# Kernel tuning notes

Hardware: AMD Instinct MI355X
Metric: run time of the kernel (lower is better)

## Reference

```python
import jax, jax.numpy as jnp
import numpy as np

B, S, D, P, W = 16, 100, 8192, 100, 3  # batch, seq, feat dim, proj width, window size


def setup_inputs() -> dict:
    key = jax.random.key(0)
    ks = jax.random.split(key, 6)
    return {
        "x": jax.random.normal(ks[0], (B, S, D), dtype=jnp.float32),
        "wq": jax.random.normal(ks[1], (D, P), dtype=jnp.float32) * (1.0 / np.sqrt(D)),
        "wk": jax.random.normal(ks[2], (D, P), dtype=jnp.float32) * (1.0 / np.sqrt(D)),
        "wv": jax.random.normal(ks[3], (D, P), dtype=jnp.float32) * (1.0 / np.sqrt(D)),
        "forwardpad": jax.random.normal(ks[4], (B, 1, D), dtype=jnp.float32),
        "backwardpad": jax.random.normal(ks[5], (B, 1, D), dtype=jnp.float32),
    }


def reference(x, wq, wk, wv, forwardpad, backwardpad):
    # pad: (B, S+2, D)
    padded = jnp.concatenate([forwardpad, x, backwardpad], axis=1)
    # gather all 100 overlapping size-3 windows at once: (B, S, W, D)
    idx = jnp.arange(S)[:, None] + jnp.arange(W)[None, :]  # (S, W)
    windows = padded[:, idx, :]
    # shared projections across all windows (original recomputed per window)
    q = jnp.einsum("bswd,dp->bswp", windows, wq)
    k = jnp.einsum("bswd,dp->bswp", windows, wk)
    v = jnp.einsum("bswd,dp->bswp", windows, wv)
    # per-window 3x3 attention
    scores = jnp.einsum("bswp,bsup->bswu", q, k)  # (B, S, W, W)
    attn = jax.nn.softmax(scores, axis=-1)
    out = jnp.einsum("bswu,bsup->bswp", attn, v)  # (B, S, W, P)
    # original concatenates windows along seq then takes [:, 1::3, :] -> center token of each window
    return out[:, :, 1, :]  # (B, S, P)
```

## Files before the change

kernel.cpp:

```cpp
#include <hip/hip_runtime.h>
#include <hip/hip_bf16.h>
#include <hip/hip_fp16.h>

constexpr int Dk   = 8192;
constexpr int Bb   = 16;
constexpr int Ss   = 100;
constexpr int Pp   = 100;
constexpr int MROW = 1632;
constexpr int NT   = 20;
constexpr int NCC  = 320;
constexpr int NQ   = 304;
constexpr int KG   = 1024;
constexpr int KC   = 16;
constexpr int CH   = 5;
constexpr int MBL  = 52;

constexpr size_t B_SEG   = (size_t)NT * KG * 128;
constexpr size_t PSTRIDE = (size_t)1664 * NCC;

typedef short s8v __attribute__((ext_vector_type(8)));
typedef short s4v __attribute__((ext_vector_type(4)));
typedef float f4v __attribute__((ext_vector_type(4)));

__device__ inline unsigned short f2bf_rne(float f) {
    unsigned u = __float_as_uint(f);
    u += 0x7fffu + ((u >> 16) & 1u);
    return (unsigned short)(u >> 16);
}

__global__ __launch_bounds__(256) void pack_b(
    const float* __restrict__ wq, const float* __restrict__ wk,
    const float* __restrict__ wv,
    short* __restrict__ b_hi, short* __restrict__ b_lo) {
    const int id = blockIdx.x * 256 + threadIdx.x;
    const int n  = id % NCC;
    const int kg = id / NCC;
    if (kg >= KG) return;

    const float* w = nullptr; int p = 0;
    if (n < 100)      { w = wq; p = n; }
    else if (n < 200) { w = wk; p = n - 100; }
    else if (n < 300) { w = wv; p = n - 200; }

    s8v hi, lo;
    #pragma unroll
    for (int j = 0; j < 8; ++j) {
        const float v = w ? w[(size_t)(kg * 8 + j) * Pp + p] : 0.0f;
        const unsigned u = __float_as_uint(v);
        hi[j] = (short)(unsigned short)(u >> 16);
        const float hf = __uint_as_float(u & 0xffff0000u);
        lo[j] = (short)f2bf_rne(v - hf);
    }
    const size_t doff = ((size_t)(n >> 4) * KG + kg) * 128 + (size_t)(n & 15) * 8;
    *(s8v*)(b_hi + doff) = hi;
    *(s8v*)(b_lo + doff) = lo;
}

__global__ __launch_bounds__(256, 2) void qkv_gemm(
    const float* __restrict__ x, const float* __restrict__ fpad,
    const float* __restrict__ bpad,
    const short* __restrict__ b_hi, const short* __restrict__ b_lo,
    unsigned short* __restrict__ part) {
    __shared__ __align__(16) short ahis[2][1024];
    __shared__ __align__(16) short alos[2][1024];

    const int mb   = blockIdx.x;
    const int kc   = blockIdx.y;
    const int tid  = threadIdx.x;
    const int w    = tid >> 6;
    const int l    = tid & 63;
    const int m    = l & 15;
    const int quad = l >> 4;

    const int sr  = tid >> 3;
    const int skq = tid & 7;
    const float* sp;
    {
        const int r = mb * 32 + sr;
        if (r >= MROW) sp = fpad;
        else {
            const int b = r / 102, rr = r - b * 102;
            if (rr == 0)        sp = fpad + (size_t)b * Dk;
            else if (rr == 101) sp = bpad + (size_t)b * Dk;
            else                sp = x + ((size_t)b * Ss + (rr - 1)) * Dk;
        }
        sp += kc * 512 + skq * 4;
    }
    const int woff = ((sr >> 4) * 4 + (skq >> 1)) * 128 + (sr & 15) * 8 + (skq & 1) * 4;

    float4 av[4];
    #pragma unroll
    for (int p = 0; p < 4; ++p) av[p] = *(const float4*)(sp + p * 32);

    s8v bh[2][5], bl[2][5];
    {
        const int kg0 = kc * 64 + quad;
        #pragma unroll
        for (int j = 0; j < 5; ++j) {
            const size_t bo = ((size_t)(w * 5 + j) * KG + kg0) * 128 + (size_t)m * 8;
            bh[0][j] = *(const s8v*)(b_hi + bo);
            bl[0][j] = *(const s8v*)(b_lo + bo);
        }
    }

    f4v acc[2][5];
    #pragma unroll
    for (int i = 0; i < 2; ++i)
        #pragma unroll
        for (int j = 0; j < 5; ++j) {
            f4v z = {0.f, 0.f, 0.f, 0.f};
            acc[i][j] = z;
        }

    #pragma unroll
    for (int s = 0; s < 16; ++s) {
        const int cur = s & 1, nxt = cur ^ 1;

        if (s < 15) {
            const int kgn = kc * 64 + (s + 1) * 4 + quad;
            #pragma unroll
            for (int j = 0; j < 5; ++j) {
                const size_t bo = ((size_t)(w * 5 + j) * KG + kgn) * 128 + (size_t)m * 8;
                bh[nxt][j] = *(const s8v*)(b_hi + bo);
                bl[nxt][j] = *(const s8v*)(b_lo + bo);
            }
        }

        const float4 va = av[s & 3];
        const float vv[4] = {va.x, va.y, va.z, va.w};
        s4v h4, l4;
        #pragma unroll
        for (int jj = 0; jj < 4; ++jj) {
            const unsigned u = __float_as_uint(vv[jj]);
            h4[jj] = (short)(unsigned short)(u >> 16);
            l4[jj] = (short)f2bf_rne(vv[jj] - __uint_as_float(u & 0xffff0000u));
        }
        if (s < 12) av[s & 3] = *(const float4*)(sp + (s + 4) * 32);

        *(s4v*)&ahis[cur][woff] = h4;
        *(s4v*)&alos[cur][woff] = l4;
        __syncthreads();

        const s8v ah0 = *(const s8v*)&ahis[cur][(quad * 16 + m) * 8];
        const s8v ah1 = *(const s8v*)&ahis[cur][((4 + quad) * 16 + m) * 8];
        const s8v al0 = *(const s8v*)&alos[cur][(quad * 16 + m) * 8];
        const s8v al1 = *(const s8v*)&alos[cur][((4 + quad) * 16 + m) * 8];

        #pragma unroll
        for (int j = 0; j < 5; ++j) {
            const s8v bhv = bh[cur][j], blv = bl[cur][j];
            acc[0][j] = __builtin_amdgcn_mfma_f32_16x16x32_bf16(ah0, bhv, acc[0][j], 0, 0, 0);
            acc[1][j] = __builtin_amdgcn_mfma_f32_16x16x32_bf16(ah1, bhv, acc[1][j], 0, 0, 0);
            acc[0][j] = __builtin_amdgcn_mfma_f32_16x16x32_bf16(al0, bhv, acc[0][j], 0, 0, 0);
            acc[1][j] = __builtin_amdgcn_mfma_f32_16x16x32_bf16(al1, bhv, acc[1][j], 0, 0, 0);
            acc[0][j] = __builtin_amdgcn_mfma_f32_16x16x32_bf16(ah0, blv, acc[0][j], 0, 0, 0);
            acc[1][j] = __builtin_amdgcn_mfma_f32_16x16x32_bf16(ah1, blv, acc[1][j], 0, 0, 0);
        }
    }

    unsigned short* __restrict__ pout = part + (size_t)kc * PSTRIDE;
    #pragma unroll
    for (int i = 0; i < 2; ++i) {
        #pragma unroll
        for (int j = 0; j < 5; ++j) {
            const int col  = (w * 5 + j) * 16 + m;
            const int row0 = mb * 32 + i * 16 + quad * 4;
            #pragma unroll
            for (int r = 0; r < 4; ++r)
                pout[(size_t)(row0 + r) * NCC + col] =
                    __half_as_ushort(__float2half(acc[i][j][r]));
        }
    }
}

__global__ __launch_bounds__(256) void reduce_k(
    const unsigned short* __restrict__ part, float* __restrict__ qkv) {
    const int t = blockIdx.x * 256 + threadIdx.x;
    const int row = t / 40;
    const int col0 = (t - row * 40) * 8;
    const size_t base = (size_t)row * NCC + col0;

    float sum[8] = {0.f, 0.f, 0.f, 0.f, 0.f, 0.f, 0.f, 0.f};
    #pragma unroll
    for (int k = 0; k < KC; ++k) {
        const s8v u = *(const s8v*)(part + (size_t)k * PSTRIDE + base);
        #pragma unroll
        for (int ii = 0; ii < 8; ++ii)
            sum[ii] += __half2float(__ushort_as_half((unsigned short)u[ii]));
    }
    if (col0 < NQ) {
        f4v a = {sum[0], sum[1], sum[2], sum[3]};
        f4v b = {sum[4], sum[5], sum[6], sum[7]};
        *(f4v*)(qkv + (size_t)row * NQ + col0)     = a;
        *(f4v*)(qkv + (size_t)row * NQ + col0 + 4) = b;
    }
}

__global__ __launch_bounds__(256) void attn3(
    const float* __restrict__ qkv, float* __restrict__ out) {
    const int blk = blockIdx.x;
    const int b  = blk / (Ss / CH);
    const int c  = blk % (Ss / CH);
    const int s0 = c * CH;
    const int tid = threadIdx.x;

    __shared__ float red[CH + 2][304];
    __shared__ float sc[CH][3];

    for (int idx = tid; idx < (CH + 2) * 300; idx += 256) {
        const int row = idx / 300, col = idx % 300;
        red[row][col] = qkv[(size_t)(b * 102 + s0 + row) * NQ + col];
    }
    __syncthreads();

    if (tid < CH * 3 * 16) {
        const int d = tid >> 4, g = tid & 15;
        const int ss = d / 3, u = d % 3;
        float ps = 0.0f;
        #pragma unroll
        for (int t = 0; t < 7; ++t) {
            const int p = g + t * 16;
            if (p < Pp) ps += red[ss + 1][p] * red[ss + u][100 + p];
        }
        #pragma unroll
        for (int off = 8; off > 0; off >>= 1) ps += __shfl_down(ps, off, 16);
        if (g == 0) sc[ss][u] = ps;
    }
    __syncthreads();

    for (int idx = tid; idx < CH * Pp; idx += 256) {
        const int ss = idx / Pp, p = idx % Pp;
        const float a0 = sc[ss][0], a1 = sc[ss][1], a2 = sc[ss][2];
        const float mx = fmaxf(a0, fmaxf(a1, a2));
        const float e0 = __expf(a0 - mx), e1 = __expf(a1 - mx), e2 = __expf(a2 - mx);
        const float inv = 1.0f / (e0 + e1 + e2);
        out[(size_t)(b * Ss + s0 + ss) * Pp + p] =
            inv * (e0 * red[ss][200 + p] + e1 * red[ss + 1][200 + p] +
                   e2 * red[ss + 2][200 + p]);
    }
}

extern "C" void kernel_launch(void* const* d_in, const int* in_sizes, int n_in,
                              void* d_out, int out_size, void* d_ws, size_t ws_size,
                              hipStream_t stream) {
    const float* x    = (const float*)d_in[0];
    const float* wq   = (const float*)d_in[1];
    const float* wk   = (const float*)d_in[2];
    const float* wv   = (const float*)d_in[3];
    const float* fpad = (const float*)d_in[4];
    const float* bpad = (const float*)d_in[5];
    float* out = (float*)d_out;

    short* b_hi = (short*)d_ws;
    short* b_lo = b_hi + B_SEG;
    unsigned short* part = (unsigned short*)(b_lo + B_SEG);
    float* qkv = (float*)(part + (size_t)KC * PSTRIDE);

    pack_b<<<(NCC * KG) / 256, 256, 0, stream>>>(wq, wk, wv, b_hi, b_lo);
    qkv_gemm<<<dim3(MBL, KC), 256, 0, stream>>>(x, fpad, bpad, b_hi, b_lo, part);
    reduce_k<<<260, 256, 0, stream>>>(part, qkv);
    attn3<<<Bb * (Ss / CH), 256, 0, stream>>>(qkv, out);
}
```

Baseline: 141.5 us.

## Vectorize weight packing, batch GEMM A staging, split reduction across lanes

pack_b now has each thread load float4s and pack four output columns, which cuts scalar global loads. qkv_gemm stages four K-steps of A into a larger LDS buffer per barrier, so it syncs less often, and it loads B fragments directly instead of double-buffering them in registers. reduce_k splits the 16-way K reduction across 4 lanes and combines them with xor shuffles, giving more threads and more memory parallelism. attn3 loads qkv with float4. The trade-offs are higher LDS use in the GEMM and the loss of B prefetch overlap.

```diff
diff --git a/kernel.cpp b/kernel.cpp
--- a/kernel.cpp
+++ b/kernel.cpp
@@ -33,27 +33,42 @@
     const float* __restrict__ wv,
     short* __restrict__ b_hi, short* __restrict__ b_lo) {
     const int id = blockIdx.x * 256 + threadIdx.x;
-    const int n  = id % NCC;
-    const int kg = id / NCC;
+    const int ng = id % 80;
+    const int kg = id / 80;
     if (kg >= KG) return;
-
-    const float* w = nullptr; int p = 0;
-    if (n < 100)      { w = wq; p = n; }
-    else if (n < 200) { w = wk; p = n - 100; }
-    else if (n < 300) { w = wv; p = n - 200; }
-
-    s8v hi, lo;
+    const int n0 = ng * 4;
+
+    const float* w = nullptr; int p0 = 0;
+    if (n0 < 100)      { w = wq; p0 = n0; }
+    else if (n0 < 200) { w = wk; p0 = n0 - 100; }
+    else if (n0 < 300) { w = wv; p0 = n0 - 200; }
+
+    float4 vj[8];
     #pragma unroll
     for (int j = 0; j < 8; ++j) {
-        const float v = w ? w[(size_t)(kg * 8 + j) * Pp + p] : 0.0f;
-        const unsigned u = __float_as_uint(v);
-        hi[j] = (short)(unsigned short)(u >> 16);
-        const float hf = __uint_as_float(u & 0xffff0000u);
-        lo[j] = (short)f2bf_rne(v - hf);
-    }
-    const size_t doff = ((size_t)(n >> 4) * KG + kg) * 128 + (size_t)(n & 15) * 8;
-    *(s8v*)(b_hi + doff) = hi;
-    *(s8v*)(b_lo + doff) = lo;
+        if (w) vj[j] = *(const float4*)(w + (size_t)(kg * 8 + j) * Pp + p0);
+        else   vj[j] = make_float4(0.f, 0.f, 0.f, 0.f);
+    }
+
+    #pragma unroll
+    for (int t = 0; t < 4; ++t) {
+        const int n = n0 + t;
+        const float vv[8] = {vj[0].x + 0.f, vj[1].x, vj[2].x, vj[3].x,
+                             vj[4].x, vj[5].x, vj[6].x, vj[7].x};
+        s8v hi, lo;
+        #pragma unroll
+        for (int j = 0; j < 8; ++j) {
+            const float v = (t == 0) ? (&vj[j].x)[0] : (t == 1) ? (&vj[j].x)[1]
+                          : (t == 2) ? (&vj[j].x)[2] : (&vj[j].x)[3];
+            const unsigned u = __float_as_uint(v);
+            hi[j] = (short)(unsigned short)(u >> 16);
+            lo[j] = (short)f2bf_rne(v - __uint_as_float(u & 0xffff0000u));
+        }
+        (void)vv;
+        const size_t doff = ((size_t)(n >> 4) * KG + kg) * 128 + (size_t)(n & 15) * 8;
+        *(s8v*)(b_hi + doff) = hi;
+        *(s8v*)(b_lo + doff) = lo;
+    }
 }
 
 __global__ __launch_bounds__(256, 2) void qkv_gemm(
@@ -61,8 +76,8 @@
     const float* __restrict__ bpad,
     const short* __restrict__ b_hi, const short* __restrict__ b_lo,
     unsigned short* __restrict__ part) {
-    __shared__ __align__(16) short ahis[2][1024];
-    __shared__ __align__(16) short alos[2][1024];
+    __shared__ __align__(16) short ahis[2][4096];
+    __shared__ __align__(16) short alos[2][4096];
 
     const int mb   = blockIdx.x;
     const int kc   = blockIdx.y;
@@ -88,21 +103,6 @@
     }
     const int woff = ((sr >> 4) * 4 + (skq >> 1)) * 128 + (sr & 15) * 8 + (skq & 1) * 4;
 
-    float4 av[4];
-    #pragma unroll
-    for (int p = 0; p < 4; ++p) av[p] = *(const float4*)(sp + p * 32);
-
-    s8v bh[2][5], bl[2][5];
-    {
-        const int kg0 = kc * 64 + quad;
-        #pragma unroll
-        for (int j = 0; j < 5; ++j) {
-            const size_t bo = ((size_t)(w * 5 + j) * KG + kg0) * 128 + (size_t)m * 8;
-            bh[0][j] = *(const s8v*)(b_hi + bo);
-            bl[0][j] = *(const s8v*)(b_lo + bo);
-        }
-    }
-
     f4v acc[2][5];
     #pragma unroll
     for (int i = 0; i < 2; ++i)
@@ -112,50 +112,58 @@
             acc[i][j] = z;
         }
 
-    #pragma unroll
-    for (int s = 0; s < 16; ++s) {
-        const int cur = s & 1, nxt = cur ^ 1;
-
-        if (s < 15) {
-            const int kgn = kc * 64 + (s + 1) * 4 + quad;
+    float4 avA[4];
+    #pragma unroll
+    for (int st = 0; st < 4; ++st) avA[st] = *(const float4*)(sp + st * 32);
+
+    #pragma unroll
+    for (int g = 0; g < 4; ++g) {
+        const int buf = g & 1;
+
+        #pragma unroll
+        for (int st = 0; st < 4; ++st) {
+            const float vv[4] = {avA[st].x, avA[st].y, avA[st].z, avA[st].w};
+            s4v h4, l4;
+            #pragma unroll
+            for (int jj = 0; jj < 4; ++jj) {
+                const unsigned u = __float_as_uint(vv[jj]);
+                h4[jj] = (short)(unsigned short)(u >> 16);
+                l4[jj] = (short)f2bf_rne(vv[jj] - __uint_as_float(u & 0xffff0000u));
+            }
+            *(s4v*)&ahis[buf][st * 1024 + woff] = h4;
+            *(s4v*)&alos[buf][st * 1024 + woff] = l4;
+        }
+        __syncthreads();
+
+        if (g < 3) {
+            #pragma unroll
+            for (int st = 0; st < 4; ++st)
+                avA[st] = *(const float4*)(sp + (g + 1) * 128 + st * 32);
+        }
+
+        #pragma unroll
+        for (int st = 0; st < 4; ++st) {
+            const int so = st * 1024;
+            const s8v ah0 = *(const s8v*)&ahis[buf][so + (quad * 16 + m) * 8];
+            const s8v ah1 = *(const s8v*)&ahis[buf][so + ((4 + quad) * 16 + m) * 8];
+            const s8v al0 = *(const s8v*)&alos[buf][so + (quad * 16 + m) * 8];
+            const s8v al1 = *(const s8v*)&alos[buf][so + ((4 + quad) * 16 + m) * 8];
+
+            const int kg = kc * 64 + g * 16 + st * 4 + quad;
             #pragma unroll
             for (int j = 0; j < 5; ++j) {
-                const size_t bo = ((size_t)(w * 5 + j) * KG + kgn) * 128 + (size_t)m * 8;
-                bh[nxt][j] = *(const s8v*)(b_hi + bo);
-                bl[nxt][j] = *(const s8v*)(b_lo + bo);
+                const size_t bo = ((size_t)(w * 5 + j) * KG + kg) * 128 + (size_t)m * 8;
+                const s8v bh = *(const s8v*)(b_hi + bo);
+                const s8v bl = *(const s8v*)(b_lo + bo);
+                acc[0][j] = __builtin_amdgcn_mfma_f32_16x16x32_bf16(ah0, bh, acc[0][j], 0, 0, 0);
+                acc[1][j] = __builtin_amdgcn_mfma_f32_16x16x32_bf16(ah1, bh, acc[1][j], 0, 0, 0);
+                acc[0][j] = __builtin_amdgcn_mfma_f32_16x16x32_bf16(al0, bh, acc[0][j], 0, 0, 0);
+                acc[1][j] = __builtin_amdgcn_mfma_f32_16x16x32_bf16(al1, bh, acc[1][j], 0, 0, 0);
+                acc[0][j] = __builtin_amdgcn_mfma_f32_16x16x32_bf16(ah0, bl, acc[0][j], 0, 0, 0);
+                acc[1][j] = __builtin_amdgcn_mfma_f32_16x16x32_bf16(ah1, bl, acc[1][j], 0, 0, 0);
             }
         }
-
-        const float4 va = av[s & 3];
-        const float vv[4] = {va.x, va.y, va.z, va.w};
-        s4v h4, l4;
-        #pragma unroll
-        for (int jj = 0; jj < 4; ++jj) {
-            const unsigned u = __float_as_uint(vv[jj]);
-            h4[jj] = (short)(unsigned short)(u >> 16);
-            l4[jj] = (short)f2bf_rne(vv[jj] - __uint_as_float(u & 0xffff0000u));
-        }
-        if (s < 12) av[s & 3] = *(const float4*)(sp + (s + 4) * 32);
-
-        *(s4v*)&ahis[cur][woff] = h4;
-        *(s4v*)&alos[cur][woff] = l4;
         __syncthreads();
-
-        const s8v ah0 = *(const s8v*)&ahis[cur][(quad * 16 + m) * 8];
-        const s8v ah1 = *(const s8v*)&ahis[cur][((4 + quad) * 16 + m) * 8];
-        const s8v al0 = *(const s8v*)&alos[cur][(quad * 16 + m) * 8];
-        const s8v al1 = *(const s8v*)&alos[cur][((4 + quad) * 16 + m) * 8];
-
-        #pragma unroll
-        for (int j = 0; j < 5; ++j) {
-            const s8v bhv = bh[cur][j], blv = bl[cur][j];
-            acc[0][j] = __builtin_amdgcn_mfma_f32_16x16x32_bf16(ah0, bhv, acc[0][j], 0, 0, 0);
-            acc[1][j] = __builtin_amdgcn_mfma_f32_16x16x32_bf16(ah1, bhv, acc[1][j], 0, 0, 0);
-            acc[0][j] = __builtin_amdgcn_mfma_f32_16x16x32_bf16(al0, bhv, acc[0][j], 0, 0, 0);
-            acc[1][j] = __builtin_amdgcn_mfma_f32_16x16x32_bf16(al1, bhv, acc[1][j], 0, 0, 0);
-            acc[0][j] = __builtin_amdgcn_mfma_f32_16x16x32_bf16(ah0, blv, acc[0][j], 0, 0, 0);
-            acc[1][j] = __builtin_amdgcn_mfma_f32_16x16x32_bf16(ah1, blv, acc[1][j], 0, 0, 0);
-        }
     }
 
     unsigned short* __restrict__ pout = part + (size_t)kc * PSTRIDE;
@@ -175,20 +183,27 @@
 
 __global__ __launch_bounds__(256) void reduce_k(
     const unsigned short* __restrict__ part, float* __restrict__ qkv) {
-    const int t = blockIdx.x * 256 + threadIdx.x;
-    const int row = t / 40;
-    const int col0 = (t - row * 40) * 8;
+    const int id = blockIdx.x * 256 + threadIdx.x;
+    const int cell = id >> 2, kq = id & 3;
+    const int row = cell / 40, c8 = cell - row * 40;
+    const int col0 = c8 * 8;
     const size_t base = (size_t)row * NCC + col0;
 
     float sum[8] = {0.f, 0.f, 0.f, 0.f, 0.f, 0.f, 0.f, 0.f};
     #pragma unroll
-    for (int k = 0; k < KC; ++k) {
-        const s8v u = *(const s8v*)(part + (size_t)k * PSTRIDE + base);
+    for (int k4 = 0; k4 < 4; ++k4) {
+        const s8v u = *(const s8v*)(part + (size_t)(kq * 4 + k4) * PSTRIDE + base);
         #pragma unroll
         for (int ii = 0; ii < 8; ++ii)
             sum[ii] += __half2float(__ushort_as_half((unsigned short)u[ii]));
     }
-    if (col0 < NQ) {
+    #pragma unroll
+    for (int mask = 1; mask < 4; mask <<= 1)
+        #pragma unroll
+        for (int ii = 0; ii < 8; ++ii)
+            sum[ii] += __shfl_xor(sum[ii], mask);
+
+    if (kq == 0 && col0 < NQ) {
         f4v a = {sum[0], sum[1], sum[2], sum[3]};
         f4v b = {sum[4], sum[5], sum[6], sum[7]};
         *(f4v*)(qkv + (size_t)row * NQ + col0)     = a;
@@ -207,9 +222,10 @@
     __shared__ float red[CH + 2][304];
     __shared__ float sc[CH][3];
 
-    for (int idx = tid; idx < (CH + 2) * 300; idx += 256) {
-        const int row = idx / 300, col = idx % 300;
-        red[row][col] = qkv[(size_t)(b * 102 + s0 + row) * NQ + col];
+    for (int idx = tid; idx < (CH + 2) * 76; idx += 256) {
+        const int row = idx / 76, cg = idx % 76;
+        *(f4v*)&red[row][cg * 4] =
+            *(const f4v*)(qkv + (size_t)(b * 102 + s0 + row) * NQ + cg * 4);
     }
     __syncthreads();
 
@@ -256,8 +272,8 @@
     unsigned short* part = (unsigned short*)(b_lo + B_SEG);
     float* qkv = (float*)(part + (size_t)KC * PSTRIDE);
 
-    pack_b<<<(NCC * KG) / 256, 256, 0, stream>>>(wq, wk, wv, b_hi, b_lo);
+    pack_b<<<(KG * 80 + 255) / 256, 256, 0, stream>>>(wq, wk, wv, b_hi, b_lo);
     qkv_gemm<<<dim3(MBL, KC), 256, 0, stream>>>(x, fpad, bpad, b_hi, b_lo, part);
-    reduce_k<<<260, 256, 0, stream>>>(part, qkv);
+    reduce_k<<<(1664 * 40 * 4) / 256, 256, 0, stream>>>(part, qkv);
     attn3<<<Bb * (Ss / CH), 256, 0, stream>>>(qkv, out);
 }
```

After: 159.6 us. +12.8%, slower.
